# Optimization experiments

Measured on AMD Instinct MI355X. Metric: run time of the kernel, lower is better.

Reference implementation:

```python
import jax, jax.numpy as jnp
import numpy as np

B, T, H, V = 64, 48, 512, 32000


def _uni(k, shape, fan_in):
    s = 1.0 / np.sqrt(fan_in)
    return jax.random.uniform(k, shape, jnp.float32, -s, s)


def setup_inputs() -> dict:
    key = jax.random.key(0)
    ks = jax.random.split(key, 21)
    inp = {
        "feat": jax.random.normal(ks[0], (B, T, H), jnp.float32),
        "caption": jax.random.normal(ks[1], (B, T, H), jnp.float32),
        "ids": jax.random.randint(ks[2], (B, T), 0, V),
    }
    i = 3
    for name, in_dim in (("1", H), ("2", 2 * H), ("d1", H), ("d2", 2 * H)):
        inp["w_ih" + name] = _uni(ks[i], (4 * H, in_dim), H); i += 1
        inp["w_hh" + name] = _uni(ks[i], (4 * H, H), H); i += 1
        inp["b_ih" + name] = _uni(ks[i], (4 * H,), H); i += 1
        inp["b_hh" + name] = _uni(ks[i], (4 * H,), H); i += 1
    inp["w_o"] = _uni(ks[i], (V, H), H); i += 1
    inp["b_o"] = _uni(ks[i], (V,), H)
    return inp


def lstm_cell(x, h, c, w_ih, w_hh, b_ih, b_hh):
    # PyTorch LSTMCell: gates in i, f, g, o order
    g = x @ w_ih.T + b_ih + h @ w_hh.T + b_hh
    gi, gf, gg, go = jnp.split(g, 4, axis=-1)
    c_new = jax.nn.sigmoid(gf) * c + jax.nn.sigmoid(gi) * jnp.tanh(gg)
    h_new = jax.nn.sigmoid(go) * jnp.tanh(c_new)
    return h_new, c_new


def reference(feat, caption, ids,
              w_ih1, w_hh1, b_ih1, b_hh1,
              w_ih2, w_hh2, b_ih2, b_hh2,
              w_ihd1, w_hhd1, b_ihd1, b_hhd1,
              w_ihd2, w_hhd2, b_ihd2, b_hhd2,
              w_o, b_o):
    pad = jnp.zeros((B, H), feat.dtype)
    z = jnp.zeros((B, H), feat.dtype)

    def enc_step(carry, x):
        h1, c1, h2, c2 = carry
        h1, c1 = lstm_cell(x, h1, c1, w_ih1, w_hh1, b_ih1, b_hh1)
        h2, c2 = lstm_cell(jnp.concatenate([pad, h1], 1), h2, c2,
                           w_ih2, w_hh2, b_ih2, b_hh2)
        return (h1, c1, h2, c2), None

    carry, _ = jax.lax.scan(enc_step, (z, z, z, z), jnp.swapaxes(feat, 0, 1))

    def dec_step(carry, xs):
        h1, c1, h2, c2 = carry
        cap, tgt = xs
        h1, c1 = lstm_cell(pad, h1, c1, w_ihd1, w_hhd1, b_ihd1, b_hhd1)
        h2, c2 = lstm_cell(jnp.concatenate([cap, h1], 1), h2, c2,
                           w_ihd2, w_hhd2, b_ihd2, b_hhd2)
        logits = h2 @ w_o.T + b_o  # [B, V]
        lp = jax.nn.log_softmax(logits, axis=-1)
        ce = -jnp.take_along_axis(lp, tgt[:, None], axis=1)[:, 0].mean()
        return (h1, c1, h2, c2), ce

    caps = jnp.swapaxes(caption[:, : T - 1, :], 0, 1)  # [T-1, B, H]
    tgts = jnp.swapaxes(ids[:, 1:T], 0, 1)             # [T-1, B]
    _, ces = jax.lax.scan(dec_step, carry, (caps, tgts))
    # total_loss += sum(mean_ce) / batch_size (word_loss is already a mean)
    return jnp.sum(ces) / B
```

## Files before the change

kernel.cpp:

```cpp
#include <hip/hip_runtime.h>
#include <math.h>

#define B_ 64
#define T_ 48
#define H_ 512
#define V_ 32000
#define G_ 2048
#define BH_ (B_*H_)
#define BG_ (B_*G_)
#define NCE_ 208

typedef short short8 __attribute__((ext_vector_type(8)));
typedef float f32x4 __attribute__((ext_vector_type(4)));

__device__ __forceinline__ float sigmoidf_(float x){ return 1.f/(1.f+__expf(-x)); }

__device__ __forceinline__ unsigned short f2bf(float f){
  unsigned u = __float_as_uint(f);
  u += 0x7fffu + ((u>>16)&1u);
  return (unsigned short)(u>>16);
}
__device__ __forceinline__ float bf2f(unsigned short u){
  return __uint_as_float(((unsigned)u)<<16);
}

__device__ __forceinline__ short8 cvt8(const float* g){
  float4 a = *(const float4*)g;
  float4 b = *(const float4*)(g+4);
  short8 v;
  v[0]=(short)f2bf(a.x); v[1]=(short)f2bf(a.y); v[2]=(short)f2bf(a.z); v[3]=(short)f2bf(a.w);
  v[4]=(short)f2bf(b.x); v[5]=(short)f2bf(b.y); v[6]=(short)f2bf(b.z); v[7]=(short)f2bf(b.w);
  return v;
}

#define F1_(i)   ((i)*16)
#define GO_(i)   ((32+(i))*16)
#define CEGO_(i) ((64+(i))*16)

__global__ void init_kernel(unsigned short* h1_0, unsigned short* h2_0, unsigned* flags){
  int i = blockIdx.x*256 + threadIdx.x;
  short8 z = {0,0,0,0,0,0,0,0};
  if (i < 4096) ((short8*)h1_0)[i] = z;
  else          ((short8*)h2_0)[i-4096] = z;
  if (i < 4352) flags[i] = 0u;
}

__global__ void cvt_cat_kernel(const float* __restrict__ s0, int ld0, int off0,
                               const float* __restrict__ s1, int ld1, int off1,
                               unsigned short* __restrict__ dst, int dld, long total8)
{
  int cols8 = dld >> 3;
  for (long i = blockIdx.x*256 + threadIdx.x; i < total8; i += (long)gridDim.x*256){
    int r = (int)(i / cols8);
    int k = (int)(i - (long)r*cols8) * 8;
    short8 v = (k < 512 || !s1) ? cvt8(s0 + (long)r*ld0 + off0 + k)
                                : cvt8(s1 + (long)r*ld1 + off1 + (k-512));
    *(short8*)(dst + (long)r*dld + k) = v;
  }
}

__global__ void bias_sum_kernel(const float* a1, const float* a2, float* o1,
                                const float* b1, const float* b2, float* o2){
  int n = blockIdx.x*256 + threadIdx.x;
  if (n < G_){ o1[n] = a1[n] + a2[n]; o2[n] = b1[n] + b2[n]; }
}

__global__ __launch_bounds__(512,1) void mm_pre_kernel(
    const float* __restrict__ A, int a_bstride,
    const unsigned short* __restrict__ Wbf,
    const float* __restrict__ bA, const float* __restrict__ bB,
    unsigned short* __restrict__ out)
{
  const int s = blockIdx.x, n0 = blockIdx.y*256;
  const int t = threadIdx.x, w = t>>6, l = t&63, ln = l&15, lk = l>>4;
  __shared__ short8 smA[64*64];
  __shared__ short8 smB[256*8];

  const float* af32 = A + (long)s*H_;

  f32x4 acc[4][2];
#pragma unroll
  for (int mf=0; mf<4; ++mf)
#pragma unroll
    for (int nf=0; nf<2; ++nf) acc[mf][nf] = (f32x4){0.f,0.f,0.f,0.f};

#pragma unroll
  for (int i=0;i<8;++i){ int e=i*4096+t*8; int m=e>>9, k=e&511;
    smA[m*64 + ((k>>3)^(m&7))] = cvt8(&af32[(long)m*a_bstride + k]); }

  for (int kc=0; kc<8; ++kc){
    __syncthreads();
#pragma unroll
    for (int i=0;i<4;++i){ int e=i*4096+t*8; int n=e>>6, k=e&63;
      smB[n*8 + ((k>>3)^(n&7))] = *(const short8*)(Wbf + (long)(n0+n)*512 + kc*64 + k); }
    __syncthreads();
#pragma unroll
    for (int ks2=0; ks2<2; ++ks2){
#pragma unroll
      for (int nf=0; nf<2; ++nf){
        int n = w*32 + nf*16 + ln;
        short8 bfr = smB[n*8 + ((ks2*4+lk)^(n&7))];
#pragma unroll
        for (int mf=0; mf<4; ++mf){
          int m = mf*16+ln;
          short8 afr = smA[m*64 + (((kc*2+ks2)*4+lk)^(m&7))];
          acc[mf][nf] = __builtin_amdgcn_mfma_f32_16x16x32_bf16(afr, bfr, acc[mf][nf], 0,0,0);
        }
      }
    }
  }
#pragma unroll
  for (int nf=0; nf<2; ++nf){
    int n = n0 + w*32 + nf*16 + ln;
    float bias = bA[n] + bB[n];
#pragma unroll
    for (int mf=0; mf<4; ++mf)
#pragma unroll
      for (int r=0; r<4; ++r){
        int m = mf*16 + lk*4 + r;
        out[(long)s*BG_ + (long)m*G_ + n] = f2bf(acc[mf][nf][r] + bias);
      }
  }
}

__global__ __launch_bounds__(256,1) void mega_kernel(
    const unsigned short* __restrict__ w1e, const unsigned short* __restrict__ w1d,
    const unsigned short* __restrict__ w2e, const unsigned short* __restrict__ w2d,
    const unsigned short* __restrict__ x1b,
    const unsigned short* __restrict__ capqb,
    const float* __restrict__ bd1s, const float* __restrict__ b2es,
    unsigned short* __restrict__ h1, unsigned short* __restrict__ h2,
    const float* __restrict__ w_o, const float* __restrict__ b_o, const int* __restrict__ ids,
    float* __restrict__ partial, float* __restrict__ tgt,
    unsigned* __restrict__ flags)
{
  __shared__ short8 smA[64*128];
  __shared__ float gbuf[4][16][68];
  __shared__ float c1_lds[16][68];
  __shared__ float c2_lds[16][68];
  const int bc = blockIdx.x;
  const int t = threadIdx.x;
  const int wv = t>>6, l = t&63, ln = l&15, lk = l>>4;

  if (bc < 32){
    const int cb = bc;
    unsigned short* stash = (unsigned short*)&smA[0];
    short8 W1e_[16], W1d_[16], W2_[32];
    const int col = wv*512 + cb*16 + ln;
    {
      const long wr1 = (long)col * 512;
#pragma unroll
      for (int ks=0; ks<16; ++ks){
        W1e_[ks] = *(const short8*)(w1e + wr1 + ks*32 + lk*8);
        W1d_[ks] = *(const short8*)(w1d + wr1 + ks*32 + lk*8);
      }
      const long wr2 = (long)col * 1024;
#pragma unroll
      for (int ks=0; ks<32; ++ks)
        W2_[ks] = *(const short8*)(w2e + wr2 + ks*32 + lk*8);
    }
    const float b1d = bd1s[col], b2e = b2es[col];

    for (int i=t; i<16*68; i+=256){ (&c1_lds[0][0])[i] = 0.f; (&c2_lds[0][0])[i] = 0.f; }
    __syncthreads();

    for (int u=0; u<96; ++u){
      if (u == 49){
        const long wr2 = (long)col * 1024;
#pragma unroll
        for (int ks=0; ks<32; ++ks)
          W2_[ks] = *(const short8*)(w2d + wr2 + ks*32 + lk*8);
      }
      const int L1a = (u<=94), L2a = (u>=1);

      float prev1[4][4], prev2[4][4];
      if (L1a){
        if (u < 48){
          const unsigned short* pp = x1b + (long)u*BG_ + col;
#pragma unroll
          for (int mf=0;mf<4;++mf)
#pragma unroll
            for (int r=0;r<4;++r) prev1[mf][r] = bf2f(pp[(long)(mf*16+lk*4+r)*G_]);
        } else {
#pragma unroll
          for (int mf=0;mf<4;++mf)
#pragma unroll
            for (int r=0;r<4;++r) prev1[mf][r] = b1d;
        }
      }
      if (L2a){
        if (u-1 < 48){
#pragma unroll
          for (int mf=0;mf<4;++mf)
#pragma unroll
            for (int r=0;r<4;++r) prev2[mf][r] = b2e;
        } else {
          const unsigned short* pp = capqb + (long)(u-1-48)*BG_ + col;
#pragma unroll
          for (int mf=0;mf<4;++mf)
#pragma unroll
            for (int r=0;r<4;++r) prev2[mf][r] = bf2f(pp[(long)(mf*16+lk*4+r)*G_]);
        }
      }

      { const unsigned short* hpB = h1 + (long)u*BH_;
#pragma unroll
        for (int i=0;i<16;++i){ int e=i*2048+t*8; int m=e>>9, k=e&511;
          smA[m*128 + ((k>>3)^(m&7)) + 64] = *(const short8*)(hpB + m*512 + k); }
        if (L2a){
          const unsigned short* hpA = h2 + (long)(u-1)*BH_;
#pragma unroll
          for (int i=0;i<16;++i){ int e=i*2048+t*8; int m=e>>9, k=e&511;
            smA[m*128 + ((k>>3)^(m&7))] = *(const short8*)(hpA + m*512 + k); }
        }
      }
      __syncthreads();

      f32x4 acc1[4], acc2[4];
      if (L1a){
#pragma unroll
        for (int mf=0;mf<4;++mf) acc1[mf] = (f32x4){0.f,0.f,0.f,0.f};
        if (u < 48){
#pragma unroll
          for (int ks=0; ks<16; ++ks)
#pragma unroll
            for (int mf=0; mf<4; ++mf){
              int m = mf*16+ln;
              acc1[mf] = __builtin_amdgcn_mfma_f32_16x16x32_bf16(
                smA[m*128 + 64 + ((ks*4+lk)^(m&7))], W1e_[ks], acc1[mf], 0,0,0);
            }
        } else {
#pragma unroll
          for (int ks=0; ks<16; ++ks)
#pragma unroll
            for (int mf=0; mf<4; ++mf){
              int m = mf*16+ln;
              acc1[mf] = __builtin_amdgcn_mfma_f32_16x16x32_bf16(
                smA[m*128 + 64 + ((ks*4+lk)^(m&7))], W1d_[ks], acc1[mf], 0,0,0);
            }
        }
#pragma unroll
        for (int mf=0;mf<4;++mf)
#pragma unroll
          for (int r=0;r<4;++r) acc1[mf][r] += prev1[mf][r];
      }
      if (L2a){
#pragma unroll
        for (int mf=0;mf<4;++mf) acc2[mf] = (f32x4){0.f,0.f,0.f,0.f};
#pragma unroll
        for (int ks=0; ks<32; ++ks)
#pragma unroll
          for (int mf=0; mf<4; ++mf){
            int m = mf*16+ln;
            acc2[mf] = __builtin_amdgcn_mfma_f32_16x16x32_bf16(
              smA[m*128 + ((ks*4+lk)^(m&7))], W2_[ks], acc2[mf], 0,0,0);
          }
#pragma unroll
        for (int mf=0;mf<4;++mf)
#pragma unroll
          for (int r=0;r<4;++r) acc2[mf][r] += prev2[mf][r];
      }

      if (L1a){
#pragma unroll
        for (int mf=0;mf<4;++mf) *(f32x4*)&gbuf[wv][ln][mf*16+lk*4] = acc1[mf];
      }
      __syncthreads();
      if (L1a){
        int n = t&15, m0 = (t>>4)*4;
        float4 gi = *(float4*)&gbuf[0][n][m0];
        float4 gf = *(float4*)&gbuf[1][n][m0];
        float4 gg = *(float4*)&gbuf[2][n][m0];
        float4 go = *(float4*)&gbuf[3][n][m0];
        float4 c4 = *(float4*)&c1_lds[n][m0];
        float a_i[4]={gi.x,gi.y,gi.z,gi.w}, a_f[4]={gf.x,gf.y,gf.z,gf.w};
        float a_g[4]={gg.x,gg.y,gg.z,gg.w}, a_o[4]={go.x,go.y,go.z,go.w};
        float ci[4]={c4.x,c4.y,c4.z,c4.w}, cn[4];
#pragma unroll
        for (int j=0;j<4;++j){
          float i_ = sigmoidf_(a_i[j]), f_ = sigmoidf_(a_f[j]), o_ = sigmoidf_(a_o[j]);
          float g_ = tanhf(a_g[j]);
          cn[j] = f_*ci[j] + i_*g_;
          stash[(m0+j)*24 + n] = f2bf(o_*tanhf(cn[j]));
        }
        *(float4*)&c1_lds[n][m0] = make_float4(cn[0],cn[1],cn[2],cn[3]);
      }
      __syncthreads();
      if (L1a){
        unsigned short* ho = h1 + (long)(u+1)*BH_ + cb*16;
        int m = t>>2, q = t&3;
        unsigned long long v = *(const unsigned long long*)&stash[m*24 + q*4];
        __hip_atomic_store((unsigned long long*)(ho + (long)m*512 + q*4), v,
                           __ATOMIC_RELAXED, __HIP_MEMORY_SCOPE_AGENT);
      }
      __syncthreads();

      if (L2a){
#pragma unroll
        for (int mf=0;mf<4;++mf) *(f32x4*)&gbuf[wv][ln][mf*16+lk*4] = acc2[mf];
      }
      __syncthreads();
      if (L2a){
        int n = t&15, m0 = (t>>4)*4;
        float4 gi = *(float4*)&gbuf[0][n][m0];
        float4 gf = *(float4*)&gbuf[1][n][m0];
        float4 gg = *(float4*)&gbuf[2][n][m0];
        float4 go = *(float4*)&gbuf[3][n][m0];
        float4 c4 = *(float4*)&c2_lds[n][m0];
        float a_i[4]={gi.x,gi.y,gi.z,gi.w}, a_f[4]={gf.x,gf.y,gf.z,gf.w};
        float a_g[4]={gg.x,gg.y,gg.z,gg.w}, a_o[4]={go.x,go.y,go.z,go.w};
        float ci[4]={c4.x,c4.y,c4.z,c4.w}, cn[4];
#pragma unroll
        for (int j=0;j<4;++j){
          float i_ = sigmoidf_(a_i[j]), f_ = sigmoidf_(a_f[j]), o_ = sigmoidf_(a_o[j]);
          float g_ = tanhf(a_g[j]);
          cn[j] = f_*ci[j] + i_*g_;
          stash[(m0+j)*24 + n] = f2bf(o_*tanhf(cn[j]));
        }
        *(float4*)&c2_lds[n][m0] = make_float4(cn[0],cn[1],cn[2],cn[3]);
      }
      __syncthreads();
      if (L2a){
        unsigned short* ho = h2 + (long)u*BH_ + cb*16;
        int m = t>>2, q = t&3;
        unsigned long long v = *(const unsigned long long*)&stash[m*24 + q*4];
        __hip_atomic_store((unsigned long long*)(ho + (long)m*512 + q*4), v,
                           __ATOMIC_RELAXED, __HIP_MEMORY_SCOPE_AGENT);
      }

      {
        unsigned g = (unsigned)(u+1);
        __syncthreads();
        if (t == 0)
          __hip_atomic_store(&flags[F1_(cb)], g, __ATOMIC_RELAXED, __HIP_MEMORY_SCOPE_AGENT);
        if (cb == 0){
          if (t < 32)
            while (__hip_atomic_load(&flags[F1_(t)], __ATOMIC_RELAXED, __HIP_MEMORY_SCOPE_AGENT) < g)
              __builtin_amdgcn_s_sleep(1);
          __syncthreads();
          if (t >= 1 && t < 32)
            __hip_atomic_store(&flags[GO_(t)], g, __ATOMIC_RELAXED, __HIP_MEMORY_SCOPE_AGENT);
          else if (t >= 32 && t < 32+NCE_)
            __hip_atomic_store(&flags[CEGO_(t-32)], g, __ATOMIC_RELAXED, __HIP_MEMORY_SCOPE_AGENT);
        } else {
          if (u < 95){
            if (t == 0)
              while (__hip_atomic_load(&flags[GO_(cb)], __ATOMIC_RELAXED, __HIP_MEMORY_SCOPE_AGENT) < g)
                __builtin_amdgcn_s_sleep(1);
          }
          __syncthreads();
        }
      }
    }
  } else {
    const int ceid = bc - 32;
    short8* smB = (short8*)&gbuf[0][0][0];
    float (*red)[64] = (float(*)[64])&c1_lds[0][0];
    int* tid_s = (int*)&c2_lds[0][0];

    for (int g2 = ceid; g2 < 47*250; g2 += NCE_){
      int td = g2 / 250, vt = g2 - td*250, v0 = vt*128;
      if (t == 0){
        unsigned need = (unsigned)(50 + td);
        while (__hip_atomic_load(&flags[CEGO_(ceid)], __ATOMIC_RELAXED, __HIP_MEMORY_SCOPE_AGENT) < need)
          __builtin_amdgcn_s_sleep(8);
      }
      __syncthreads();

      if (t < 64) tid_s[t] = ids[t*T_ + td + 1];
      { const unsigned short* hp = h2 + (long)(49+td)*BH_;
#pragma unroll
        for (int i=0;i<16;++i){ int e=i*2048+t*8; int m=e>>9, k=e&511;
          smA[m*64 + ((k>>3)^(m&7))] = *(const short8*)(hp + m*512 + k); } }

      f32x4 acc[4][2];
#pragma unroll
      for (int mf=0; mf<4; ++mf)
#pragma unroll
        for (int nf=0; nf<2; ++nf) acc[mf][nf] = (f32x4){0.f,0.f,0.f,0.f};

      for (int kc=0; kc<8; ++kc){
        __syncthreads();
#pragma unroll
        for (int i=0;i<4;++i){ int e=i*2048+t*8; int n=e>>6, k=e&63;
          smB[n*8 + ((k>>3)^(n&7))] = cvt8(&w_o[(long)(v0+n)*512 + kc*64 + k]); }
        __syncthreads();
#pragma unroll
        for (int ks2=0; ks2<2; ++ks2){
#pragma unroll
          for (int nf=0; nf<2; ++nf){
            int n = wv*32 + nf*16 + ln;
            short8 bfr = smB[n*8 + ((ks2*4+lk)^(n&7))];
#pragma unroll
            for (int mf=0; mf<4; ++mf){
              int m = mf*16+ln;
              short8 afr = smA[m*64 + (((kc*2+ks2)*4+lk)^(m&7))];
              acc[mf][nf] = __builtin_amdgcn_mfma_f32_16x16x32_bf16(afr, bfr, acc[mf][nf], 0,0,0);
            }
          }
        }
      }

      float se[4][4];
#pragma unroll
      for (int mf=0; mf<4; ++mf)
#pragma unroll
        for (int r=0;r<4;++r) se[mf][r] = 0.f;
#pragma unroll
      for (int nf=0; nf<2; ++nf){
        int ng = v0 + wv*32 + nf*16 + ln;
        float bo = b_o[ng];
#pragma unroll
        for (int mf=0; mf<4; ++mf)
#pragma unroll
          for (int r=0;r<4;++r){
            int m = mf*16 + lk*4 + r;
            float lg = acc[mf][nf][r] + bo;
            se[mf][r] += __expf(lg);
            if (ng == tid_s[m]) tgt[td*64 + m] = lg;
          }
      }
#pragma unroll
      for (int off=1; off<16; off<<=1)
#pragma unroll
        for (int mf=0; mf<4; ++mf)
#pragma unroll
          for (int r=0;r<4;++r) se[mf][r] += __shfl_xor(se[mf][r], off);
      if (ln == 0){
#pragma unroll
        for (int mf=0; mf<4; ++mf)
          *(f32x4*)&red[wv][mf*16 + lk*4] = (f32x4){se[mf][0],se[mf][1],se[mf][2],se[mf][3]};
      }
      __syncthreads();
      if (t < 64){
        float ssum = red[0][t] + red[1][t] + red[2][t] + red[3][t];
        partial[(long)vt*3008 + td*64 + t] = ssum;
      }
      __syncthreads();
    }
  }
}

__global__ void ce_combine(const float* __restrict__ partial, const float* __restrict__ tgt,
                           float* __restrict__ ce_row){
  int r = blockIdx.x*256 + threadIdx.x;
  if (r < 3008){
    float s = 0.f;
    for (int i=0;i<250;++i) s += partial[(long)i*3008 + r];
    ce_row[r] = __logf(s) - tgt[r];
  }
}

__global__ void ce_final(const float* __restrict__ ce_row, float* __restrict__ out){
  __shared__ float red[256];
  float s = 0.f;
  for (int i=threadIdx.x; i<3008; i+=256) s += ce_row[i];
  red[threadIdx.x] = s;
  __syncthreads();
  for (int off=128; off>0; off>>=1){
    if (threadIdx.x < off) red[threadIdx.x] += red[threadIdx.x + off];
    __syncthreads();
  }
  if (threadIdx.x == 0) out[0] = red[0] * (1.0f/4096.0f);
}

extern "C" void kernel_launch(void* const* d_in, const int* in_sizes, int n_in,
                              void* d_out, int out_size, void* d_ws, size_t ws_size,
                              hipStream_t stream)
{
  (void)in_sizes; (void)n_in; (void)out_size; (void)ws_size;
  const float* feat    = (const float*)d_in[0];
  const float* caption = (const float*)d_in[1];
  const int*   ids     = (const int*)d_in[2];
  const float* w_ih1  = (const float*)d_in[3];
  const float* w_hh1  = (const float*)d_in[4];
  const float* b_ih1  = (const float*)d_in[5];
  const float* b_hh1  = (const float*)d_in[6];
  const float* w_ih2  = (const float*)d_in[7];
  const float* w_hh2  = (const float*)d_in[8];
  const float* b_ih2  = (const float*)d_in[9];
  const float* b_hh2  = (const float*)d_in[10];
  const float* w_hhd1 = (const float*)d_in[12];
  const float* b_ihd1 = (const float*)d_in[13];
  const float* b_hhd1 = (const float*)d_in[14];
  const float* w_ihd2 = (const float*)d_in[15];
  const float* w_hhd2 = (const float*)d_in[16];
  const float* b_ihd2 = (const float*)d_in[17];
  const float* b_hhd2 = (const float*)d_in[18];
  const float* w_o    = (const float*)d_in[19];
  const float* b_o    = (const float*)d_in[20];

  char* p = (char*)d_ws;
  unsigned short* h1    = (unsigned short*)p; p += 96L*BH_*2;
  unsigned short* h2    = (unsigned short*)p; p += 96L*BH_*2;
  unsigned short* w1e   = (unsigned short*)p; p += 2048L*512*2;
  unsigned short* w1d   = (unsigned short*)p; p += 2048L*512*2;
  unsigned short* w2e   = (unsigned short*)p; p += 2048L*1024*2;
  unsigned short* w2d   = (unsigned short*)p; p += 2048L*1024*2;
  unsigned short* wx1   = (unsigned short*)p; p += 2048L*512*2;
  unsigned short* wcap  = (unsigned short*)p; p += 2048L*512*2;
  unsigned short* x1b   = (unsigned short*)p; p += 48L*BG_*2;
  unsigned short* capqb = (unsigned short*)p; p += 47L*BG_*2;
  float* bd1s  = (float*)p; p += 2048*4;
  float* b2es  = (float*)p; p += 2048*4;
  float* partial = (float*)p; p += 250L*3008*4;
  float* tgt   = (float*)p; p += 3008*4;
  float* ce_row= (float*)p; p += 3008*4;
  unsigned* flags = (unsigned*)p; p += 4352*4;

  init_kernel<<<32, 256, 0, stream>>>(h1, h2, flags);

  cvt_cat_kernel<<<256, 256, 0, stream>>>(w_hh1, 512, 0, nullptr, 0, 0, w1e, 512, 2048L*64);
  cvt_cat_kernel<<<256, 256, 0, stream>>>(w_hhd1, 512, 0, nullptr, 0, 0, w1d, 512, 2048L*64);
  cvt_cat_kernel<<<256, 256, 0, stream>>>(w_hh2, 512, 0, w_ih2, 1024, 512, w2e, 1024, 2048L*128);
  cvt_cat_kernel<<<256, 256, 0, stream>>>(w_hhd2, 512, 0, w_ihd2, 1024, 512, w2d, 1024, 2048L*128);
  cvt_cat_kernel<<<256, 256, 0, stream>>>(w_ih1, 512, 0, nullptr, 0, 0, wx1, 512, 2048L*64);
  cvt_cat_kernel<<<256, 256, 0, stream>>>(w_ihd2, 1024, 0, nullptr, 0, 0, wcap, 512, 2048L*64);
  bias_sum_kernel<<<8, 256, 0, stream>>>(b_ihd1, b_hhd1, bd1s, b_ih2, b_hh2, b2es);

  mm_pre_kernel<<<dim3(48,8), 512, 0, stream>>>(feat, T_*H_, wx1, b_ih1, b_hh1, x1b);
  mm_pre_kernel<<<dim3(47,8), 512, 0, stream>>>(caption, T_*H_, wcap, b_ihd2, b_hhd2, capqb);

  mega_kernel<<<32+NCE_, 256, 0, stream>>>(
      w1e, w1d, w2e, w2d, x1b, capqb, bd1s, b2es, h1, h2,
      w_o, b_o, ids, partial, tgt, flags);

  ce_combine<<<12, 256, 0, stream>>>(partial, tgt, ce_row);
  ce_final<<<1, 256, 0, stream>>>(ce_row, (float*)d_out);
}
```

Baseline: 1.846 ms.

## Split mega kernel into recurrent chain and separate batched CE projection kernel

The persistent mega kernel, which ran the LSTM recurrence and overlapped the vocabulary projection and cross-entropy in spare blocks, is replaced. A chain kernel on 32 blocks now runs only the recurrence, and a later 250-block kernel computes the logits and softmax partial sums against a w_o converted once to bf16 in a fused prep kernel. The setup launches (weight conversions, bias sums, init) and the two input projection GEMMs are each merged into single launches. This removes the per-tile fp32-to-bf16 conversion of w_o and the flag polling between CE blocks and the chain, but gives up overlapping the CE work with the serial recurrence.

Measured after the change: 2.110 ms. 1.14x slower.

```diff
diff --git a/kernel.cpp b/kernel.cpp
--- a/kernel.cpp
+++ b/kernel.cpp
@@ -8,7 +8,6 @@
 #define G_ 2048
 #define BH_ (B_*H_)
 #define BG_ (B_*G_)
-#define NCE_ 208
 
 typedef short short8 __attribute__((ext_vector_type(8)));
 typedef float f32x4 __attribute__((ext_vector_type(4)));
@@ -33,50 +32,69 @@
   return v;
 }
 
-#define F1_(i)   ((i)*16)
-#define GO_(i)   ((32+(i))*16)
-#define CEGO_(i) ((64+(i))*16)
-
-__global__ void init_kernel(unsigned short* h1_0, unsigned short* h2_0, unsigned* flags){
-  int i = blockIdx.x*256 + threadIdx.x;
-  short8 z = {0,0,0,0,0,0,0,0};
-  if (i < 4096) ((short8*)h1_0)[i] = z;
-  else          ((short8*)h2_0)[i-4096] = z;
-  if (i < 4352) flags[i] = 0u;
-}
-
-__global__ void cvt_cat_kernel(const float* __restrict__ s0, int ld0, int off0,
-                               const float* __restrict__ s1, int ld1, int off1,
-                               unsigned short* __restrict__ dst, int dld, long total8)
+__global__ void prep_kernel(
+    const float* __restrict__ w_hh1, const float* __restrict__ w_hhd1,
+    const float* __restrict__ w_hh2, const float* __restrict__ w_ih2,
+    const float* __restrict__ w_hhd2, const float* __restrict__ w_ihd2,
+    const float* __restrict__ w_ih1, const float* __restrict__ w_o,
+    const float* __restrict__ b_ihd1, const float* __restrict__ b_hhd1,
+    const float* __restrict__ b_ih2,  const float* __restrict__ b_hh2,
+    unsigned short* w1e, unsigned short* w1d, unsigned short* w2e, unsigned short* w2d,
+    unsigned short* wx1, unsigned short* wcap, unsigned short* wo_bf,
+    float* bd1s, float* b2es,
+    unsigned short* h1_0, unsigned short* h2_0, unsigned* flags)
 {
-  int cols8 = dld >> 3;
-  for (long i = blockIdx.x*256 + threadIdx.x; i < total8; i += (long)gridDim.x*256){
-    int r = (int)(i / cols8);
-    int k = (int)(i - (long)r*cols8) * 8;
-    short8 v = (k < 512 || !s1) ? cvt8(s0 + (long)r*ld0 + off0 + k)
-                                : cvt8(s1 + (long)r*ld1 + off1 + (k-512));
-    *(short8*)(dst + (long)r*dld + k) = v;
-  }
-}
-
-__global__ void bias_sum_kernel(const float* a1, const float* a2, float* o1,
-                                const float* b1, const float* b2, float* o2){
-  int n = blockIdx.x*256 + threadIdx.x;
-  if (n < G_){ o1[n] = a1[n] + a2[n]; o2[n] = b1[n] + b2[n]; }
-}
-
-__global__ __launch_bounds__(512,1) void mm_pre_kernel(
-    const float* __restrict__ A, int a_bstride,
-    const unsigned short* __restrict__ Wbf,
-    const float* __restrict__ bA, const float* __restrict__ bB,
-    unsigned short* __restrict__ out)
+  const int b = blockIdx.x, t = threadIdx.x;
+  if (b < 64){
+    for (long i = b*256+t; i < 2048L*64; i += 64L*256){ int r=(int)(i>>6), k=(int)(i&63)*8;
+      *(short8*)(w1e + (long)r*512 + k) = cvt8(w_hh1 + (long)r*512 + k); }
+  } else if (b < 128){
+    for (long i = (b-64)*256+t; i < 2048L*64; i += 64L*256){ int r=(int)(i>>6), k=(int)(i&63)*8;
+      *(short8*)(w1d + (long)r*512 + k) = cvt8(w_hhd1 + (long)r*512 + k); }
+  } else if (b < 256){
+    for (long i = (b-128)*256+t; i < 2048L*128; i += 128L*256){ int r=(int)(i>>7), k=(int)(i&127)*8;
+      short8 v = (k<512)? cvt8(w_hh2+(long)r*512+k) : cvt8(w_ih2+(long)r*1024+512+(k-512));
+      *(short8*)(w2e + (long)r*1024 + k) = v; }
+  } else if (b < 384){
+    for (long i = (b-256)*256+t; i < 2048L*128; i += 128L*256){ int r=(int)(i>>7), k=(int)(i&127)*8;
+      short8 v = (k<512)? cvt8(w_hhd2+(long)r*512+k) : cvt8(w_ihd2+(long)r*1024+512+(k-512));
+      *(short8*)(w2d + (long)r*1024 + k) = v; }
+  } else if (b < 448){
+    for (long i = (b-384)*256+t; i < 2048L*64; i += 64L*256){ int r=(int)(i>>6), k=(int)(i&63)*8;
+      *(short8*)(wx1 + (long)r*512 + k) = cvt8(w_ih1 + (long)r*512 + k); }
+  } else if (b < 512){
+    for (long i = (b-448)*256+t; i < 2048L*64; i += 64L*256){ int r=(int)(i>>6), k=(int)(i&63)*8;
+      *(short8*)(wcap + (long)r*512 + k) = cvt8(w_ihd2 + (long)r*1024 + k); }
+  } else if (b < 1012){
+    for (long i = (long)(b-512)*256+t; i < 32000L*64; i += 500L*256){ int r=(int)(i>>6), k=(int)(i&63)*8;
+      *(short8*)(wo_bf + (long)r*512 + k) = cvt8(w_o + (long)r*512 + k); }
+  } else if (b < 1020){
+    int n = (b-1012)*256 + t;
+    bd1s[n] = b_ihd1[n] + b_hhd1[n];
+    b2es[n] = b_ih2[n] + b_hh2[n];
+  } else {
+    short8 z = {0,0,0,0,0,0,0,0};
+    for (int i=(b-1020)*256+t; i<4096; i+=4*256){ ((short8*)h1_0)[i]=z; ((short8*)h2_0)[i]=z; }
+    for (int i=(b-1020)*256+t; i<4096; i+=4*256) flags[i] = 0u;
+  }
+}
+
+__global__ __launch_bounds__(512,1) void mm_pre2_kernel(
+    const float* __restrict__ feat, const float* __restrict__ caption,
+    const unsigned short* __restrict__ wx1, const unsigned short* __restrict__ wcap,
+    const float* __restrict__ b_ih1, const float* __restrict__ b_hh1,
+    const float* __restrict__ b_ihd2, const float* __restrict__ b_hhd2,
+    unsigned short* __restrict__ x1b, unsigned short* __restrict__ capqb)
 {
   const int s = blockIdx.x, n0 = blockIdx.y*256;
   const int t = threadIdx.x, w = t>>6, l = t&63, ln = l&15, lk = l>>4;
   __shared__ short8 smA[64*64];
   __shared__ short8 smB[256*8];
 
-  const float* af32 = A + (long)s*H_;
+  const float* af32; const unsigned short* Wbf; const float* bA; const float* bB;
+  unsigned short* out;
+  if (s < 48){ af32 = feat + (long)s*H_;          Wbf = wx1;  bA = b_ih1;  bB = b_hh1;  out = x1b  + (long)s*BG_; }
+  else       { af32 = caption + (long)(s-48)*H_;  Wbf = wcap; bA = b_ihd2; bB = b_hhd2; out = capqb + (long)(s-48)*BG_; }
 
   f32x4 acc[4][2];
 #pragma unroll
@@ -86,7 +104,7 @@
 
 #pragma unroll
   for (int i=0;i<8;++i){ int e=i*4096+t*8; int m=e>>9, k=e&511;
-    smA[m*64 + ((k>>3)^(m&7))] = cvt8(&af32[(long)m*a_bstride + k]); }
+    smA[m*64 + ((k>>3)^(m&7))] = cvt8(&af32[(long)m*(T_*H_) + k]); }
 
   for (int kc=0; kc<8; ++kc){
     __syncthreads();
@@ -118,325 +136,298 @@
 #pragma unroll
       for (int r=0; r<4; ++r){
         int m = mf*16 + lk*4 + r;
-        out[(long)s*BG_ + (long)m*G_ + n] = f2bf(acc[mf][nf][r] + bias);
-      }
-  }
-}
-
-__global__ __launch_bounds__(256,1) void mega_kernel(
+        out[(long)m*G_ + n] = f2bf(acc[mf][nf][r] + bias);
+      }
+  }
+}
+
+__global__ __launch_bounds__(256,1) void chain_kernel(
     const unsigned short* __restrict__ w1e, const unsigned short* __restrict__ w1d,
     const unsigned short* __restrict__ w2e, const unsigned short* __restrict__ w2d,
-    const unsigned short* __restrict__ x1b,
-    const unsigned short* __restrict__ capqb,
+    const unsigned short* __restrict__ x1b, const unsigned short* __restrict__ capqb,
     const float* __restrict__ bd1s, const float* __restrict__ b2es,
     unsigned short* __restrict__ h1, unsigned short* __restrict__ h2,
-    const float* __restrict__ w_o, const float* __restrict__ b_o, const int* __restrict__ ids,
-    float* __restrict__ partial, float* __restrict__ tgt,
     unsigned* __restrict__ flags)
 {
   __shared__ short8 smA[64*128];
   __shared__ float gbuf[4][16][68];
   __shared__ float c1_lds[16][68];
   __shared__ float c2_lds[16][68];
-  const int bc = blockIdx.x;
+  const int cb = blockIdx.x;
   const int t = threadIdx.x;
   const int wv = t>>6, l = t&63, ln = l&15, lk = l>>4;
-
-  if (bc < 32){
-    const int cb = bc;
-    unsigned short* stash = (unsigned short*)&smA[0];
-    short8 W1e_[16], W1d_[16], W2_[32];
-    const int col = wv*512 + cb*16 + ln;
-    {
-      const long wr1 = (long)col * 512;
-#pragma unroll
-      for (int ks=0; ks<16; ++ks){
-        W1e_[ks] = *(const short8*)(w1e + wr1 + ks*32 + lk*8);
-        W1d_[ks] = *(const short8*)(w1d + wr1 + ks*32 + lk*8);
-      }
+  unsigned short* stash = (unsigned short*)&smA[0];
+
+  short8 W1e_[16], W1d_[16], W2_[32];
+  const int col = wv*512 + cb*16 + ln;
+  {
+    const long wr1 = (long)col * 512;
+#pragma unroll
+    for (int ks=0; ks<16; ++ks){
+      W1e_[ks] = *(const short8*)(w1e + wr1 + ks*32 + lk*8);
+      W1d_[ks] = *(const short8*)(w1d + wr1 + ks*32 + lk*8);
+    }
+    const long wr2 = (long)col * 1024;
+#pragma unroll
+    for (int ks=0; ks<32; ++ks)
+      W2_[ks] = *(const short8*)(w2e + wr2 + ks*32 + lk*8);
+  }
+  const float b1d = bd1s[col], b2e = b2es[col];
+
+  for (int i=t; i<16*68; i+=256){ (&c1_lds[0][0])[i] = 0.f; (&c2_lds[0][0])[i] = 0.f; }
+  __syncthreads();
+
+  for (int u=0; u<96; ++u){
+    if (u == 49){
       const long wr2 = (long)col * 1024;
 #pragma unroll
       for (int ks=0; ks<32; ++ks)
-        W2_[ks] = *(const short8*)(w2e + wr2 + ks*32 + lk*8);
-    }
-    const float b1d = bd1s[col], b2e = b2es[col];
-
-    for (int i=t; i<16*68; i+=256){ (&c1_lds[0][0])[i] = 0.f; (&c2_lds[0][0])[i] = 0.f; }
-    __syncthreads();
-
-    for (int u=0; u<96; ++u){
-      if (u == 49){
-        const long wr2 = (long)col * 1024;
-#pragma unroll
-        for (int ks=0; ks<32; ++ks)
-          W2_[ks] = *(const short8*)(w2d + wr2 + ks*32 + lk*8);
-      }
-      const int L1a = (u<=94), L2a = (u>=1);
-
-      float prev1[4][4], prev2[4][4];
-      if (L1a){
-        if (u < 48){
-          const unsigned short* pp = x1b + (long)u*BG_ + col;
-#pragma unroll
-          for (int mf=0;mf<4;++mf)
-#pragma unroll
-            for (int r=0;r<4;++r) prev1[mf][r] = bf2f(pp[(long)(mf*16+lk*4+r)*G_]);
-        } else {
-#pragma unroll
-          for (int mf=0;mf<4;++mf)
-#pragma unroll
-            for (int r=0;r<4;++r) prev1[mf][r] = b1d;
-        }
-      }
+        W2_[ks] = *(const short8*)(w2d + wr2 + ks*32 + lk*8);
+    }
+    const int L1a = (u<=94), L2a = (u>=1);
+
+    float prev1[4][4], prev2[4][4];
+    if (L1a){
+      if (u < 48){
+        const unsigned short* pp = x1b + (long)u*BG_ + col;
+#pragma unroll
+        for (int mf=0;mf<4;++mf)
+#pragma unroll
+          for (int r=0;r<4;++r) prev1[mf][r] = bf2f(pp[(long)(mf*16+lk*4+r)*G_]);
+      } else {
+#pragma unroll
+        for (int mf=0;mf<4;++mf)
+#pragma unroll
+          for (int r=0;r<4;++r) prev1[mf][r] = b1d;
+      }
+    }
+    if (L2a){
+      if (u-1 < 48){
+#pragma unroll
+        for (int mf=0;mf<4;++mf)
+#pragma unroll
+          for (int r=0;r<4;++r) prev2[mf][r] = b2e;
+      } else {
+        const unsigned short* pp = capqb + (long)(u-1-48)*BG_ + col;
+#pragma unroll
+        for (int mf=0;mf<4;++mf)
+#pragma unroll
+          for (int r=0;r<4;++r) prev2[mf][r] = bf2f(pp[(long)(mf*16+lk*4+r)*G_]);
+      }
+    }
+
+    { const unsigned short* hpB = h1 + (long)u*BH_;
+#pragma unroll
+      for (int i=0;i<16;++i){ int e=i*2048+t*8; int m=e>>9, k=e&511;
+        smA[m*128 + ((k>>3)^(m&7)) + 64] = *(const short8*)(hpB + m*512 + k); }
       if (L2a){
-        if (u-1 < 48){
-#pragma unroll
-          for (int mf=0;mf<4;++mf)
-#pragma unroll
-            for (int r=0;r<4;++r) prev2[mf][r] = b2e;
-        } else {
-          const unsigned short* pp = capqb + (long)(u-1-48)*BG_ + col;
-#pragma unroll
-          for (int mf=0;mf<4;++mf)
-#pragma unroll
-            for (int r=0;r<4;++r) prev2[mf][r] = bf2f(pp[(long)(mf*16+lk*4+r)*G_]);
-        }
-      }
-
-      { const unsigned short* hpB = h1 + (long)u*BH_;
+        const unsigned short* hpA = h2 + (long)(u-1)*BH_;
 #pragma unroll
         for (int i=0;i<16;++i){ int e=i*2048+t*8; int m=e>>9, k=e&511;
-          smA[m*128 + ((k>>3)^(m&7)) + 64] = *(const short8*)(hpB + m*512 + k); }
-        if (L2a){
-          const unsigned short* hpA = h2 + (long)(u-1)*BH_;
-#pragma unroll
-          for (int i=0;i<16;++i){ int e=i*2048+t*8; int m=e>>9, k=e&511;
-            smA[m*128 + ((k>>3)^(m&7))] = *(const short8*)(hpA + m*512 + k); }
-        }
-      }
-      __syncthreads();
-
-      f32x4 acc1[4], acc2[4];
-      if (L1a){
-#pragma unroll
-        for (int mf=0;mf<4;++mf) acc1[mf] = (f32x4){0.f,0.f,0.f,0.f};
-        if (u < 48){
-#pragma unroll
-          for (int ks=0; ks<16; ++ks)
-#pragma unroll
-            for (int mf=0; mf<4; ++mf){
-              int m = mf*16+ln;
-              acc1[mf] = __builtin_amdgcn_mfma_f32_16x16x32_bf16(
-                smA[m*128 + 64 + ((ks*4+lk)^(m&7))], W1e_[ks], acc1[mf], 0,0,0);
-            }
-        } else {
-#pragma unroll
-          for (int ks=0; ks<16; ++ks)
-#pragma unroll
-            for (int mf=0; mf<4; ++mf){
-              int m = mf*16+ln;
-              acc1[mf] = __builtin_amdgcn_mfma_f32_16x16x32_bf16(
-                smA[m*128 + 64 + ((ks*4+lk)^(m&7))], W1d_[ks], acc1[mf], 0,0,0);
-            }
-        }
-#pragma unroll
-        for (int mf=0;mf<4;++mf)
-#pragma unroll
-          for (int r=0;r<4;++r) acc1[mf][r] += prev1[mf][r];
-      }
-      if (L2a){
-#pragma unroll
-        for (int mf=0;mf<4;++mf) acc2[mf] = (f32x4){0.f,0.f,0.f,0.f};
-#pragma unroll
-        for (int ks=0; ks<32; ++ks)
+          smA[m*128 + ((k>>3)^(m&7))] = *(const short8*)(hpA + m*512 + k); }
+      }
+    }
+    __syncthreads();
+
+    f32x4 acc1[4], acc2[4];
+    if (L1a){
+#pragma unroll
+      for (int mf=0;mf<4;++mf) acc1[mf] = (f32x4){0.f,0.f,0.f,0.f};
+      if (u < 48){
+#pragma unroll
+        for (int ks=0; ks<16; ++ks)
 #pragma unroll
           for (int mf=0; mf<4; ++mf){
             int m = mf*16+ln;
-            acc2[mf] = __builtin_amdgcn_mfma_f32_16x16x32_bf16(
-              smA[m*128 + ((ks*4+lk)^(m&7))], W2_[ks], acc2[mf], 0,0,0);
+            acc1[mf] = __builtin_amdgcn_mfma_f32_16x16x32_bf16(
+              smA[m*128 + 64 + ((ks*4+lk)^(m&7))], W1e_[ks], acc1[mf], 0,0,0);
           }
-#pragma unroll
-        for (int mf=0;mf<4;++mf)
-#pragma unroll
-          for (int r=0;r<4;++r) acc2[mf][r] += prev2[mf][r];
-      }
-
-      if (L1a){
-#pragma unroll
-        for (int mf=0;mf<4;++mf) *(f32x4*)&gbuf[wv][ln][mf*16+lk*4] = acc1[mf];
-      }
+      } else {
+#pragma unroll
+        for (int ks=0; ks<16; ++ks)
+#pragma unroll
+          for (int mf=0; mf<4; ++mf){
+            int m = mf*16+ln;
+            acc1[mf] = __builtin_amdgcn_mfma_f32_16x16x32_bf16(
+              smA[m*128 + 64 + ((ks*4+lk)^(m&7))], W1d_[ks], acc1[mf], 0,0,0);
+          }
+      }
+#pragma unroll
+      for (int mf=0;mf<4;++mf)
+#pragma unroll
+        for (int r=0;r<4;++r) acc1[mf][r] += prev1[mf][r];
+    }
+    if (L2a){
+#pragma unroll
+      for (int mf=0;mf<4;++mf) acc2[mf] = (f32x4){0.f,0.f,0.f,0.f};
+#pragma unroll
+      for (int ks=0; ks<32; ++ks)
+#pragma unroll
+        for (int mf=0; mf<4; ++mf){
+          int m = mf*16+ln;
+          acc2[mf] = __builtin_amdgcn_mfma_f32_16x16x32_bf16(
+            smA[m*128 + ((ks*4+lk)^(m&7))], W2_[ks], acc2[mf], 0,0,0);
+        }
+#pragma unroll
+      for (int mf=0;mf<4;++mf)
+#pragma unroll
+        for (int r=0;r<4;++r) acc2[mf][r] += prev2[mf][r];
+    }
+
+    if (L1a){
+#pragma unroll
+      for (int mf=0;mf<4;++mf) *(f32x4*)&gbuf[wv][ln][mf*16+lk*4] = acc1[mf];
+    }
+    __syncthreads();
+    if (L1a){
+      int n = t&15, m0 = (t>>4)*4;
+      float4 gi = *(float4*)&gbuf[0][n][m0];
+      float4 gf = *(float4*)&gbuf[1][n][m0];
+      float4 gg = *(float4*)&gbuf[2][n][m0];
+      float4 go = *(float4*)&gbuf[3][n][m0];
+      float4 c4 = *(float4*)&c1_lds[n][m0];
+      float a_i[4]={gi.x,gi.y,gi.z,gi.w}, a_f[4]={gf.x,gf.y,gf.z,gf.w};
+      float a_g[4]={gg.x,gg.y,gg.z,gg.w}, a_o[4]={go.x,go.y,go.z,go.w};
+      float ci[4]={c4.x,c4.y,c4.z,c4.w}, cn[4];
+#pragma unroll
+      for (int j=0;j<4;++j){
+        float i_ = sigmoidf_(a_i[j]), f_ = sigmoidf_(a_f[j]), o_ = sigmoidf_(a_o[j]);
+        float g_ = tanhf(a_g[j]);
+        cn[j] = f_*ci[j] + i_*g_;
+        stash[(m0+j)*24 + n] = f2bf(o_*tanhf(cn[j]));
+      }
+      *(float4*)&c1_lds[n][m0] = make_float4(cn[0],cn[1],cn[2],cn[3]);
+    }
+    __syncthreads();
+    if (L1a){
+      unsigned short* ho = h1 + (long)(u+1)*BH_ + cb*16;
+      int m = t>>2, q = t&3;
+      unsigned long long v = *(const unsigned long long*)&stash[m*24 + q*4];
+      __hip_atomic_store((unsigned long long*)(ho + (long)m*512 + q*4), v,
+                         __ATOMIC_RELAXED, __HIP_MEMORY_SCOPE_AGENT);
+    }
+    __syncthreads();
+
+    if (L2a){
+#pragma unroll
+      for (int mf=0;mf<4;++mf) *(f32x4*)&gbuf[wv][ln][mf*16+lk*4] = acc2[mf];
+    }
+    __syncthreads();
+    if (L2a){
+      int n = t&15, m0 = (t>>4)*4;
+      float4 gi = *(float4*)&gbuf[0][n][m0];
+      float4 gf = *(float4*)&gbuf[1][n][m0];
+      float4 gg = *(float4*)&gbuf[2][n][m0];
+      float4 go = *(float4*)&gbuf[3][n][m0];
+      float4 c4 = *(float4*)&c2_lds[n][m0];
+      float a_i[4]={gi.x,gi.y,gi.z,gi.w}, a_f[4]={gf.x,gf.y,gf.z,gf.w};
+      float a_g[4]={gg.x,gg.y,gg.z,gg.w}, a_o[4]={go.x,go.y,go.z,go.w};
+      float ci[4]={c4.x,c4.y,c4.z,c4.w}, cn[4];
+#pragma unroll
+      for (int j=0;j<4;++j){
+        float i_ = sigmoidf_(a_i[j]), f_ = sigmoidf_(a_f[j]), o_ = sigmoidf_(a_o[j]);
+        float g_ = tanhf(a_g[j]);
+        cn[j] = f_*ci[j] + i_*g_;
+        stash[(m0+j)*24 + n] = f2bf(o_*tanhf(cn[j]));
+      }
+      *(float4*)&c2_lds[n][m0] = make_float4(cn[0],cn[1],cn[2],cn[3]);
+    }
+    __syncthreads();
+    if (L2a){
+      unsigned short* ho = h2 + (long)u*BH_ + cb*16;
+      int m = t>>2, q = t&3;
+      unsigned long long v = *(const unsigned long long*)&stash[m*24 + q*4];
+      __hip_atomic_store((unsigned long long*)(ho + (long)m*512 + q*4), v,
+                         __ATOMIC_RELAXED, __HIP_MEMORY_SCOPE_AGENT);
+    }
+
+    if (u < 95){
+      unsigned g = (unsigned)(u+1);
       __syncthreads();
-      if (L1a){
-        int n = t&15, m0 = (t>>4)*4;
-        float4 gi = *(float4*)&gbuf[0][n][m0];
-        float4 gf = *(float4*)&gbuf[1][n][m0];
-        float4 gg = *(float4*)&gbuf[2][n][m0];
-        float4 go = *(float4*)&gbuf[3][n][m0];
-        float4 c4 = *(float4*)&c1_lds[n][m0];
-        float a_i[4]={gi.x,gi.y,gi.z,gi.w}, a_f[4]={gf.x,gf.y,gf.z,gf.w};
-        float a_g[4]={gg.x,gg.y,gg.z,gg.w}, a_o[4]={go.x,go.y,go.z,go.w};
-        float ci[4]={c4.x,c4.y,c4.z,c4.w}, cn[4];
-#pragma unroll
-        for (int j=0;j<4;++j){
-          float i_ = sigmoidf_(a_i[j]), f_ = sigmoidf_(a_f[j]), o_ = sigmoidf_(a_o[j]);
-          float g_ = tanhf(a_g[j]);
-          cn[j] = f_*ci[j] + i_*g_;
-          stash[(m0+j)*24 + n] = f2bf(o_*tanhf(cn[j]));
+      if (t == 0)
+        __hip_atomic_store(&flags[cb*16], g, __ATOMIC_RELAXED, __HIP_MEMORY_SCOPE_AGENT);
+      if (t < 32){
+        while (__hip_atomic_load(&flags[t*16], __ATOMIC_RELAXED, __HIP_MEMORY_SCOPE_AGENT) < g)
+          __builtin_amdgcn_s_sleep(1);
+      }
+      __syncthreads();
+    }
+  }
+}
+
+__global__ __launch_bounds__(512,1) void ce_vt_kernel(
+    const unsigned short* __restrict__ h2_bf, const unsigned short* __restrict__ wo_bf,
+    const float* __restrict__ b_o, const int* __restrict__ ids,
+    float* __restrict__ partial, float* __restrict__ tgt)
+{
+  const int vt = blockIdx.x, v0 = vt*128;
+  const int t = threadIdx.x, wv = t>>6, l = t&63, ln = l&15, lk = l>>4;
+  __shared__ short8 smB[128*64];
+  __shared__ short8 smAc[64*8];
+  __shared__ float red[8][64];
+  __shared__ int tid_s[64];
+
+  for (int i = t; i < 128*64; i += 512){
+    int n = i >> 6, c = i & 63;
+    smB[n*64 + ((c & 56) | ((c & 7) ^ (n & 7)))] =
+        *(const short8*)(wo_bf + (long)(v0+n)*512 + c*8);
+  }
+  const int nn = wv*16 + ln;
+  const float bo = b_o[v0 + nn];
+  __syncthreads();
+
+  for (int td = 0; td < 47; ++td){
+    if (t < 64) tid_s[t] = ids[t*T_ + td + 1];
+    const unsigned short* hp = h2_bf + (long)(49+td)*BH_;
+
+    f32x4 acc[4];
+#pragma unroll
+    for (int mf=0;mf<4;++mf) acc[mf] = (f32x4){0.f,0.f,0.f,0.f};
+
+    for (int kc=0; kc<8; ++kc){
+      __syncthreads();
+      { int m = t>>3, c = t&7;
+        smAc[m*8 + (c ^ (m&7))] = *(const short8*)(hp + m*512 + kc*64 + c*8); }
+      __syncthreads();
+#pragma unroll
+      for (int ks2=0; ks2<2; ++ks2){
+        short8 bfr = smB[nn*64 + kc*8 + ((ks2*4+lk)^(nn&7))];
+#pragma unroll
+        for (int mf=0; mf<4; ++mf){
+          int m = mf*16+ln;
+          short8 afr = smAc[m*8 + ((ks2*4+lk)^(m&7))];
+          acc[mf] = __builtin_amdgcn_mfma_f32_16x16x32_bf16(afr, bfr, acc[mf], 0,0,0);
         }
-        *(float4*)&c1_lds[n][m0] = make_float4(cn[0],cn[1],cn[2],cn[3]);
-      }
-      __syncthreads();
-      if (L1a){
-        unsigned short* ho = h1 + (long)(u+1)*BH_ + cb*16;
-        int m = t>>2, q = t&3;
-        unsigned long long v = *(const unsigned long long*)&stash[m*24 + q*4];
-        __hip_atomic_store((unsigned long long*)(ho + (long)m*512 + q*4), v,
-                           __ATOMIC_RELAXED, __HIP_MEMORY_SCOPE_AGENT);
-      }
-      __syncthreads();
-
-      if (L2a){
-#pragma unroll
-        for (int mf=0;mf<4;++mf) *(f32x4*)&gbuf[wv][ln][mf*16+lk*4] = acc2[mf];
-      }
-      __syncthreads();
-      if (L2a){
-        int n = t&15, m0 = (t>>4)*4;
-        float4 gi = *(float4*)&gbuf[0][n][m0];
-        float4 gf = *(float4*)&gbuf[1][n][m0];
-        float4 gg = *(float4*)&gbuf[2][n][m0];
-        float4 go = *(float4*)&gbuf[3][n][m0];
-        float4 c4 = *(float4*)&c2_lds[n][m0];
-        float a_i[4]={gi.x,gi.y,gi.z,gi.w}, a_f[4]={gf.x,gf.y,gf.z,gf.w};
-        float a_g[4]={gg.x,gg.y,gg.z,gg.w}, a_o[4]={go.x,go.y,go.z,go.w};
-        float ci[4]={c4.x,c4.y,c4.z,c4.w}, cn[4];
-#pragma unroll
-        for (int j=0;j<4;++j){
-          float i_ = sigmoidf_(a_i[j]), f_ = sigmoidf_(a_f[j]), o_ = sigmoidf_(a_o[j]);
-          float g_ = tanhf(a_g[j]);
-          cn[j] = f_*ci[j] + i_*g_;
-          stash[(m0+j)*24 + n] = f2bf(o_*tanhf(cn[j]));
-        }
-        *(float4*)&c2_lds[n][m0] = make_float4(cn[0],cn[1],cn[2],cn[3]);
-      }
-      __syncthreads();
-      if (L2a){
-        unsigned short* ho = h2 + (long)u*BH_ + cb*16;
-        int m = t>>2, q = t&3;
-        unsigned long long v = *(const unsigned long long*)&stash[m*24 + q*4];
-        __hip_atomic_store((unsigned long long*)(ho + (long)m*512 + q*4), v,
-                           __ATOMIC_RELAXED, __HIP_MEMORY_SCOPE_AGENT);
-      }
-
-      {
-        unsigned g = (unsigned)(u+1);
-        __syncthreads();
-        if (t == 0)
-          __hip_atomic_store(&flags[F1_(cb)], g, __ATOMIC_RELAXED, __HIP_MEMORY_SCOPE_AGENT);
-        if (cb == 0){
-          if (t < 32)
-            while (__hip_atomic_load(&flags[F1_(t)], __ATOMIC_RELAXED, __HIP_MEMORY_SCOPE_AGENT) < g)
-              __builtin_amdgcn_s_sleep(1);
-          __syncthreads();
-          if (t >= 1 && t < 32)
-            __hip_atomic_store(&flags[GO_(t)], g, __ATOMIC_RELAXED, __HIP_MEMORY_SCOPE_AGENT);
-          else if (t >= 32 && t < 32+NCE_)
-            __hip_atomic_store(&flags[CEGO_(t-32)], g, __ATOMIC_RELAXED, __HIP_MEMORY_SCOPE_AGENT);
-        } else {
-          if (u < 95){
-            if (t == 0)
-              while (__hip_atomic_load(&flags[GO_(cb)], __ATOMIC_RELAXED, __HIP_MEMORY_SCOPE_AGENT) < g)
-                __builtin_amdgcn_s_sleep(1);
-          }
-          __syncthreads();
-        }
-      }
-    }
-  } else {
-    const int ceid = bc - 32;
-    short8* smB = (short8*)&gbuf[0][0][0];
-    float (*red)[64] = (float(*)[64])&c1_lds[0][0];
-    int* tid_s = (int*)&c2_lds[0][0];
-
-    for (int g2 = ceid; g2 < 47*250; g2 += NCE_){
-      int td = g2 / 250, vt = g2 - td*250, v0 = vt*128;
-      if (t == 0){
-        unsigned need = (unsigned)(50 + td);
-        while (__hip_atomic_load(&flags[CEGO_(ceid)], __ATOMIC_RELAXED, __HIP_MEMORY_SCOPE_AGENT) < need)
-          __builtin_amdgcn_s_sleep(8);
-      }
-      __syncthreads();
-
-      if (t < 64) tid_s[t] = ids[t*T_ + td + 1];
-      { const unsigned short* hp = h2 + (long)(49+td)*BH_;
-#pragma unroll
-        for (int i=0;i<16;++i){ int e=i*2048+t*8; int m=e>>9, k=e&511;
-          smA[m*64 + ((k>>3)^(m&7))] = *(const short8*)(hp + m*512 + k); } }
-
-      f32x4 acc[4][2];
+      }
+    }
+
+    float se[4][4];
+#pragma unroll
+    for (int mf=0; mf<4; ++mf)
+#pragma unroll
+      for (int r=0;r<4;++r){
+        int m = mf*16 + lk*4 + r;
+        float lg = acc[mf][r] + bo;
+        se[mf][r] = __expf(lg);
+        if (v0 + nn == tid_s[m]) tgt[td*64 + m] = lg;
+      }
+#pragma unroll
+    for (int off=1; off<16; off<<=1)
 #pragma unroll
       for (int mf=0; mf<4; ++mf)
 #pragma unroll
-        for (int nf=0; nf<2; ++nf) acc[mf][nf] = (f32x4){0.f,0.f,0.f,0.f};
-
-      for (int kc=0; kc<8; ++kc){
-        __syncthreads();
-#pragma unroll
-        for (int i=0;i<4;++i){ int e=i*2048+t*8; int n=e>>6, k=e&63;
-          smB[n*8 + ((k>>3)^(n&7))] = cvt8(&w_o[(long)(v0+n)*512 + kc*64 + k]); }
-        __syncthreads();
-#pragma unroll
-        for (int ks2=0; ks2<2; ++ks2){
-#pragma unroll
-          for (int nf=0; nf<2; ++nf){
-            int n = wv*32 + nf*16 + ln;
-            short8 bfr = smB[n*8 + ((ks2*4+lk)^(n&7))];
-#pragma unroll
-            for (int mf=0; mf<4; ++mf){
-              int m = mf*16+ln;
-              short8 afr = smA[m*64 + (((kc*2+ks2)*4+lk)^(m&7))];
-              acc[mf][nf] = __builtin_amdgcn_mfma_f32_16x16x32_bf16(afr, bfr, acc[mf][nf], 0,0,0);
-            }
-          }
-        }
-      }
-
-      float se[4][4];
+        for (int r=0;r<4;++r) se[mf][r] += __shfl_xor(se[mf][r], off);
+    if (ln == 0){
 #pragma unroll
       for (int mf=0; mf<4; ++mf)
-#pragma unroll
-        for (int r=0;r<4;++r) se[mf][r] = 0.f;
-#pragma unroll
-      for (int nf=0; nf<2; ++nf){
-        int ng = v0 + wv*32 + nf*16 + ln;
-        float bo = b_o[ng];
-#pragma unroll
-        for (int mf=0; mf<4; ++mf)
-#pragma unroll
-          for (int r=0;r<4;++r){
-            int m = mf*16 + lk*4 + r;
-            float lg = acc[mf][nf][r] + bo;
-            se[mf][r] += __expf(lg);
-            if (ng == tid_s[m]) tgt[td*64 + m] = lg;
-          }
-      }
-#pragma unroll
-      for (int off=1; off<16; off<<=1)
-#pragma unroll
-        for (int mf=0; mf<4; ++mf)
-#pragma unroll
-          for (int r=0;r<4;++r) se[mf][r] += __shfl_xor(se[mf][r], off);
-      if (ln == 0){
-#pragma unroll
-        for (int mf=0; mf<4; ++mf)
-          *(f32x4*)&red[wv][mf*16 + lk*4] = (f32x4){se[mf][0],se[mf][1],se[mf][2],se[mf][3]};
-      }
-      __syncthreads();
-      if (t < 64){
-        float ssum = red[0][t] + red[1][t] + red[2][t] + red[3][t];
-        partial[(long)vt*3008 + td*64 + t] = ssum;
-      }
-      __syncthreads();
+        *(f32x4*)&red[wv][mf*16 + lk*4] = (f32x4){se[mf][0],se[mf][1],se[mf][2],se[mf][3]};
+    }
+    __syncthreads();
+    if (t < 64){
+      float ssum = 0.f;
+#pragma unroll
+      for (int w2=0; w2<8; ++w2) ssum += red[w2][t];
+      partial[(long)vt*3008 + td*64 + t] = ssum;
     }
   }
 }
@@ -501,30 +492,26 @@
   unsigned short* wcap  = (unsigned short*)p; p += 2048L*512*2;
   unsigned short* x1b   = (unsigned short*)p; p += 48L*BG_*2;
   unsigned short* capqb = (unsigned short*)p; p += 47L*BG_*2;
+  unsigned short* wo_bf = (unsigned short*)p; p += 32000L*512*2;
   float* bd1s  = (float*)p; p += 2048*4;
   float* b2es  = (float*)p; p += 2048*4;
   float* partial = (float*)p; p += 250L*3008*4;
   float* tgt   = (float*)p; p += 3008*4;
   float* ce_row= (float*)p; p += 3008*4;
-  unsigned* flags = (unsigned*)p; p += 4352*4;
-
-  init_kernel<<<32, 256, 0, stream>>>(h1, h2, flags);
-
-  cvt_cat_kernel<<<256, 256, 0, stream>>>(w_hh1, 512, 0, nullptr, 0, 0, w1e, 512, 2048L*64);
-  cvt_cat_kernel<<<256, 256, 0, stream>>>(w_hhd1, 512, 0, nullptr, 0, 0, w1d, 512, 2048L*64);
-  cvt_cat_kernel<<<256, 256, 0, stream>>>(w_hh2, 512, 0, w_ih2, 1024, 512, w2e, 1024, 2048L*128);
-  cvt_cat_kernel<<<256, 256, 0, stream>>>(w_hhd2, 512, 0, w_ihd2, 1024, 512, w2d, 1024, 2048L*128);
-  cvt_cat_kernel<<<256, 256, 0, stream>>>(w_ih1, 512, 0, nullptr, 0, 0, wx1, 512, 2048L*64);
-  cvt_cat_kernel<<<256, 256, 0, stream>>>(w_ihd2, 1024, 0, nullptr, 0, 0, wcap, 512, 2048L*64);
-  bias_sum_kernel<<<8, 256, 0, stream>>>(b_ihd1, b_hhd1, bd1s, b_ih2, b_hh2, b2es);
-
-  mm_pre_kernel<<<dim3(48,8), 512, 0, stream>>>(feat, T_*H_, wx1, b_ih1, b_hh1, x1b);
-  mm_pre_kernel<<<dim3(47,8), 512, 0, stream>>>(caption, T_*H_, wcap, b_ihd2, b_hhd2, capqb);
-
-  mega_kernel<<<32+NCE_, 256, 0, stream>>>(
-      w1e, w1d, w2e, w2d, x1b, capqb, bd1s, b2es, h1, h2,
-      w_o, b_o, ids, partial, tgt, flags);
-
+  unsigned* flags = (unsigned*)p; p += 4096*4;
+
+  prep_kernel<<<1024, 256, 0, stream>>>(
+      w_hh1, w_hhd1, w_hh2, w_ih2, w_hhd2, w_ihd2, w_ih1, w_o,
+      b_ihd1, b_hhd1, b_ih2, b_hh2,
+      w1e, w1d, w2e, w2d, wx1, wcap, wo_bf, bd1s, b2es, h1, h2, flags);
+
+  mm_pre2_kernel<<<dim3(95,8), 512, 0, stream>>>(
+      feat, caption, wx1, wcap, b_ih1, b_hh1, b_ihd2, b_hhd2, x1b, capqb);
+
+  chain_kernel<<<32, 256, 0, stream>>>(
+      w1e, w1d, w2e, w2d, x1b, capqb, bd1s, b2es, h1, h2, flags);
+
+  ce_vt_kernel<<<250, 512, 0, stream>>>(h2, wo_bf, b_o, ids, partial, tgt);
   ce_combine<<<12, 256, 0, stream>>>(partial, tgt, ce_row);
   ce_final<<<1, 256, 0, stream>>>(ce_row, (float*)d_out);
 }
```
